# Kernel tuning notes

Measured on AMD Instinct MI355X. Metric: run time of the kernel, lower is better.

The kernel has to match this reference:

```python
import jax, jax.numpy as jnp
import numpy as np

D_MODEL = 1024
NHEAD = 16
HEAD_DIM = D_MODEL // NHEAD
SF_THRESHOLD = 4.0
SF_LEVELS = 8
STEP = SF_THRESHOLD / SF_LEVELS  # quantization step of ScaleAndFireNeuron
EPS = 1e-6


def setup_inputs() -> dict:
    key = jax.random.key(0)
    ks = jax.random.split(key, 12)
    B, L, D = 2, 2048, D_MODEL
    s = 1.0 / np.sqrt(D)
    inp = {
        "x": jax.random.normal(ks[0], (B, L, D), dtype=jnp.float32),
        "wq": jax.random.normal(ks[1], (D, D), dtype=jnp.float32) * s,
        "bq": jnp.zeros((D,), dtype=jnp.float32),
        "wk": jax.random.normal(ks[2], (D, D), dtype=jnp.float32) * s,
        "bk": jnp.zeros((D,), dtype=jnp.float32),
        "wv": jax.random.normal(ks[3], (D, D), dtype=jnp.float32) * s,
        "bv": jnp.zeros((D,), dtype=jnp.float32),
        "wo": jax.random.normal(ks[4], (D, D), dtype=jnp.float32) * s,
        "bo": jnp.zeros((D,), dtype=jnp.float32),
        "gq": jnp.ones((HEAD_DIM,), dtype=jnp.float32),  # SpikingQKNorm gain (q)
        "gk": jnp.ones((HEAD_DIM,), dtype=jnp.float32),  # SpikingQKNorm gain (k)
    }
    return inp


def _rms_norm(t, g):
    # SpikingQKNorm: RMS normalization over head_dim with learned gain
    return t * jax.lax.rsqrt(jnp.mean(t * t, axis=-1, keepdims=True) + EPS) * g


def _sfn(t):
    # ScaleAndFireNeuron: T=1 multi-level spike quantization with straight-through estimator.
    # Levels are integer multiples of STEP, clipped to +/- SF_LEVELS.
    q = jnp.clip(jnp.round(t / STEP), -SF_LEVELS, SF_LEVELS) * STEP
    return t + jax.lax.stop_gradient(q - t)


def reference(x, wq, bq, wk, bk, wv, bv, wo, bo, gq, gk):
    B, L, D = x.shape
    H, Dh = NHEAD, HEAD_DIM
    scale = Dh ** -0.5

    def proj(w, b):
        return (x @ w.T + b).reshape(B, L, H, Dh).transpose(0, 2, 1, 3)  # [B,H,L,Dh]

    q = _sfn(_rms_norm(proj(wq, bq), gq))
    k = _sfn(_rms_norm(proj(wk, bk), gk))
    v = _sfn(proj(wv, bv))

    scores = jnp.einsum('bhqd,bhkd->bhqk', q, k) * scale  # [B,H,L,L]
    probs = jax.nn.softmax(scores, axis=-1)
    out = jnp.einsum('bhqk,bhkd->bhqd', probs, v)  # [B,H,L,Dh]
    out = out.transpose(0, 2, 1, 3).reshape(B, L, D)
    return out @ wo.T + bo
```

## Files before the change

### kernel.cpp

```cpp
#include <hip/hip_runtime.h>
#include <stdint.h>

#define D_MODEL 1024
#define NHEAD 16
#define HEAD_DIM 64
#define SEQ 2048
#define BATCH 2
#define MROWS (BATCH*SEQ)
#define KVBLK 128
#define KVTILES (SEQ/KVBLK)

typedef unsigned short u16;
typedef short bf16x8 __attribute__((ext_vector_type(8)));
typedef float f32x4 __attribute__((ext_vector_type(4)));
typedef float f32x16 __attribute__((ext_vector_type(16)));

__device__ inline float bf2f(u16 h){ return __uint_as_float(((unsigned)h)<<16); }
__device__ inline u16 f2bf(float x){
  unsigned u = __float_as_uint(x);
  unsigned r = (u + 0x7FFFu + ((u>>16)&1u)) >> 16;
  return (u16)r;
}

__device__ inline f32x4 mfma_bf16(bf16x8 a, bf16x8 b, f32x4 c){
  return __builtin_amdgcn_mfma_f32_16x16x32_bf16(a, b, c, 0, 0, 0);
}
__device__ inline f32x16 mfma32_bf16(bf16x8 a, bf16x8 b, f32x16 c){
  return __builtin_amdgcn_mfma_f32_32x32x16_bf16(a, b, c, 0, 0, 0);
}

__device__ inline void gld_lds16(const u16* g, u16* l){
  __builtin_amdgcn_global_load_lds(
      (const __attribute__((address_space(1))) void*)g,
      (__attribute__((address_space(3))) void*)l, 16, 0, 0);
}

__device__ inline int swz8(int row){ return (row ^ (row >> 3)) & 7; }

__device__ inline uint32_t pack_bf2(float p0, float p1){
  uint32_t u0 = __float_as_uint(p0) + 0x8000u;
  uint32_t u1 = __float_as_uint(p1) + 0x8000u;
  return __builtin_amdgcn_perm(u1, u0, 0x07060302u);
}

__global__ __launch_bounds__(256) void pack_split(const float* __restrict__ src,
                                                  u16* __restrict__ hi, u16* __restrict__ lo, int n4){
  int i = blockIdx.x*256 + threadIdx.x;
  if (i >= n4) return;
  float4 v = ((const float4*)src)[i];
  float vv[4] = {v.x, v.y, v.z, v.w};
  u16 h[4], l[4];
  #pragma unroll
  for (int j=0;j<4;j++){
    h[j] = f2bf(vv[j]);
    l[j] = f2bf(vv[j] - bf2f(h[j]));
  }
  ((ushort4*)hi)[i] = make_ushort4(h[0],h[1],h[2],h[3]);
  ((ushort4*)lo)[i] = make_ushort4(l[0],l[1],l[2],l[3]);
}

__global__ __launch_bounds__(256) void pack_w(const float* __restrict__ wq, const float* __restrict__ wk,
                                              const float* __restrict__ wv, const float* __restrict__ wo,
                                              u16* __restrict__ qkv_hi, u16* __restrict__ qkv_lo,
                                              u16* __restrict__ wo_hi, u16* __restrict__ wo_lo){
  int which = blockIdx.x >> 10;
  int i = ((blockIdx.x & 1023) << 8) + threadIdx.x;
  const float* src = which==0 ? wq : which==1 ? wk : which==2 ? wv : wo;
  u16* hi = (which==3) ? wo_hi : qkv_hi + ((size_t)which << 20);
  u16* lo = (which==3) ? wo_lo : qkv_lo + ((size_t)which << 20);
  float4 v = ((const float4*)src)[i];
  float vv[4] = {v.x, v.y, v.z, v.w};
  u16 h[4], l[4];
  #pragma unroll
  for (int j=0;j<4;j++){
    h[j] = f2bf(vv[j]);
    l[j] = f2bf(vv[j] - bf2f(h[j]));
  }
  ((ushort4*)hi)[i] = make_ushort4(h[0],h[1],h[2],h[3]);
  ((ushort4*)lo)[i] = make_ushort4(l[0],l[1],l[2],l[3]);
}

__global__ __launch_bounds__(512) void gemm_qkv(
    const u16* __restrict__ a_hi, const u16* __restrict__ a_lo,
    const u16* __restrict__ b_hi, const u16* __restrict__ b_lo,
    const float* __restrict__ bq, const float* __restrict__ bk_,
    const float* __restrict__ bv,
    u16* __restrict__ qb, u16* __restrict__ kb, u16* __restrict__ vb,
    const float* __restrict__ gq, const float* __restrict__ gk)
{
  __shared__ u16 ldsq[4][16384];
  const int tid = threadIdx.x;
  const int lane = tid & 63;
  const int w = tid >> 6;
  const int wr = w >> 2, wc = w & 3;
  const int l15 = lane & 15;
  const int m0 = blockIdx.x * 256;
  const int n0 = blockIdx.y * 256;
  const int NT = 96;

  f32x4 acc[8][4];
  #pragma unroll
  for (int i=0;i<8;i++)
    #pragma unroll
    for (int j=0;j<4;j++) acc[i][j] = (f32x4){0.f,0.f,0.f,0.f};

  auto stageq = [&](int t){
    u16* base = &ldsq[t & 3][0];
    const u16* As = ((t>>5)==1) ? a_lo : a_hi;
    const u16* Bs = ((t>>5)==2) ? b_lo : b_hi;
    const int kk = (t & 31) << 5;
    #pragma unroll
    for (int r2=0;r2<2;r2++){
      int idx = tid + r2*512;
      int row = idx >> 2, s = idx & 3;
      int g = s ^ ((row >> 1) & 3);
      gld_lds16(As + (size_t)(m0+row)*1024 + kk + (g<<3), base + (idx<<3));
    }
    #pragma unroll
    for (int r2=0;r2<2;r2++){
      int idx = tid + r2*512;
      int row = idx >> 2, s = idx & 3;
      int g = s ^ ((row >> 1) & 3);
      gld_lds16(Bs + (size_t)(n0+row)*1024 + kk + (g<<3), base + 8192 + (idx<<3));
    }
  };

  const int slot = ((lane >> 4) ^ ((l15 >> 1) & 3)) << 3;

  stageq(0); stageq(1);
  asm volatile("s_waitcnt vmcnt(4)" ::: "memory");
  __builtin_amdgcn_s_barrier();

  for (int t=0; t<NT; ++t){
    if (t+2 < NT) stageq(t+2);
    const u16* la = &ldsq[t & 3][0];
    const u16* lb = &ldsq[t & 3][8192];
    bf16x8 af[8], bfr[4];
    #pragma unroll
    for (int mf=0;mf<8;mf++)
      af[mf] = *(const bf16x8*)&la[(wr*128 + mf*16 + l15)*32 + slot];
    #pragma unroll
    for (int nf=0;nf<4;nf++)
      bfr[nf] = *(const bf16x8*)&lb[(wc*64 + nf*16 + l15)*32 + slot];
    __builtin_amdgcn_s_setprio(1);
    #pragma unroll
    for (int mf=0;mf<8;mf++)
      #pragma unroll
      for (int nf=0;nf<4;nf++)
        acc[mf][nf] = mfma_bf16(af[mf], bfr[nf], acc[mf][nf]);
    __builtin_amdgcn_s_setprio(0);
    if (t+1 < NT){
      if (t+2 < NT) asm volatile("s_waitcnt vmcnt(4)" ::: "memory");
      else          asm volatile("s_waitcnt vmcnt(0)" ::: "memory");
      __builtin_amdgcn_s_barrier();
    }
  }

  const int gcolbase = n0 + wc*64;
  const int sidx = gcolbase >> 6;
  const int ttype = sidx < 16 ? 0 : (sidx < 32 ? 1 : 2);
  u16* dst = ttype==0 ? qb : (ttype==1 ? kb : vb);
  const float* bsrc = ttype==0 ? bq : (ttype==1 ? bk_ : bv);
  const int h = sidx - (ttype==1 ? 16 : (ttype==2 ? 32 : 0));
  float gvals[4], bvals[4];
  #pragma unroll
  for (int j=0;j<4;j++){
    int dh = j*16 + l15;
    bvals[j] = bsrc[(gcolbase & 1023) + dh];
    gvals[j] = ttype==0 ? gq[dh] : (ttype==1 ? gk[dh] : 1.0f);
  }
  #pragma unroll
  for (int mf=0;mf<8;mf++){
    #pragma unroll
    for (int r=0;r<4;r++){
      float tv[4];
      float ssq = 0.f;
      #pragma unroll
      for (int j=0;j<4;j++){ tv[j] = acc[mf][j][r] + bvals[j]; ssq += tv[j]*tv[j]; }
      ssq += __shfl_xor(ssq, 1);
      ssq += __shfl_xor(ssq, 2);
      ssq += __shfl_xor(ssq, 4);
      ssq += __shfl_xor(ssq, 8);
      float s = 1.0f;
      if (ttype < 2) s = 1.0f / sqrtf(ssq * (1.0f/64.0f) + 1e-6f);
      int row = m0 + wr*128 + mf*16 + (lane>>4)*4 + r;
      int bi = row >> 11, li = row & 2047;
      size_t obase = ((size_t)(bi*NHEAD + h)*SEQ + li)*HEAD_DIM;
      #pragma unroll
      for (int j=0;j<4;j++){
        float val = tv[j] * s * gvals[j];
        float z = rintf(val * 2.0f);
        z = fminf(8.0f, fmaxf(-8.0f, z));
        dst[obase + j*16 + l15] = f2bf(z * 0.5f);
      }
    }
  }
}

__global__ __launch_bounds__(256) void gemm_bt(
    const u16* __restrict__ a_hi, const u16* __restrict__ b_hi,
    const float* __restrict__ bias, float* __restrict__ out_f,
    int M, int N, int K)
{
  __shared__ u16 lds[2][8192];
  const int tid = threadIdx.x;
  const int lane = tid & 63;
  const int w = tid >> 6;
  const int wr = w >> 1, wc = w & 1;
  const int m0 = blockIdx.x * 128;
  const int n0 = blockIdx.y * 128;
  const int NT = K / 32;

  f32x4 acc[4][4];
  #pragma unroll
  for (int i=0;i<4;i++)
    #pragma unroll
    for (int j=0;j<4;j++) acc[i][j] = (f32x4){0.f,0.f,0.f,0.f};

  auto stage = [&](int buf, int kt){
    int kk = kt * 32;
    u16* base = &lds[buf][0];
    #pragma unroll
    for (int r=0;r<2;r++){
      const u16* g = a_hi + (size_t)(m0 + (tid>>2) + r*64)*K + kk + (tid&3)*8;
      gld_lds16(g, base + w*512 + r*2048);
    }
    #pragma unroll
    for (int r=0;r<2;r++){
      const u16* g = b_hi + (size_t)(n0 + (tid>>2) + r*64)*K + kk + (tid&3)*8;
      gld_lds16(g, base + 4096 + w*512 + r*2048);
    }
  };

  stage(0, 0);
  for (int kt=0; kt<NT; ++kt){
    __syncthreads();
    if (kt+1 < NT) stage((kt+1)&1, kt+1);
    const u16* la = &lds[kt&1][0];
    const u16* lb = &lds[kt&1][4096];
    const int koff = (lane>>4)*8;
    const int rowa = wr*64 + (lane&15);
    const int rowb = wc*64 + (lane&15);
    bf16x8 af[4], bfv[4];
    #pragma unroll
    for (int i=0;i<4;i++) af[i]  = *(const bf16x8*)&la[(rowa + i*16)*32 + koff];
    #pragma unroll
    for (int i=0;i<4;i++) bfv[i] = *(const bf16x8*)&lb[(rowb + i*16)*32 + koff];
    #pragma unroll
    for (int i=0;i<4;i++)
      #pragma unroll
      for (int j=0;j<4;j++)
        acc[i][j] = mfma_bf16(af[i], bfv[j], acc[i][j]);
  }

  const int gcolbase = n0 + wc*64;
  #pragma unroll
  for (int j=0;j<4;j++){
    float bj = bias[gcolbase + j*16 + (lane&15)];
    #pragma unroll
    for (int i=0;i<4;i++){
      int row = m0 + wr*64 + i*16 + (lane>>4)*4;
      #pragma unroll
      for (int r=0;r<4;r++)
        out_f[(size_t)(row+r)*N + gcolbase + j*16 + (lane&15)] = acc[i][j][r] + bj;
    }
  }
}

__global__ __launch_bounds__(256) void transpose_v(const u16* __restrict__ v, u16* __restrict__ vt){
  __shared__ u16 tl[64][66];
  int bh = blockIdx.x >> 5;
  int l0 = (blockIdx.x & 31) * 64;
  int tid = threadIdx.x;
  #pragma unroll
  for (int it=0; it<2; ++it){
    int idx = tid + it*256;
    int row = idx >> 3, g = idx & 7;
    bf16x8 d = *(const bf16x8*)(v + ((size_t)bh*SEQ + l0 + row)*64 + g*8);
    #pragma unroll
    for (int j=0;j<8;j++) tl[row][g*8+j] = (u16)d[j];
  }
  __syncthreads();
  #pragma unroll
  for (int it=0; it<2; ++it){
    int idx = tid + it*256;
    int dh = idx >> 3, g = idx & 7;
    u16 tmp[8];
    #pragma unroll
    for (int j=0;j<8;j++) tmp[j] = tl[g*8+j][dh];
    *(bf16x8*)(vt + ((size_t)bh*HEAD_DIM + dh)*SEQ + l0 + g*8) = *(const bf16x8*)tmp;
  }
}

__global__ __launch_bounds__(256) void attn_kernel(
    const u16* __restrict__ qb, const u16* __restrict__ kb, const u16* __restrict__ vt,
    u16* __restrict__ attn_out)
{
  __shared__ u16 lds_k[2][KVBLK*64];
  __shared__ u16 lds_v[2][64*KVBLK];
  const int tid = threadIdx.x, lane = tid & 63, w = tid >> 6;
  const int bh = blockIdx.y;
  const int q0 = blockIdx.x * 128;
  const size_t kvbase = (size_t)bh * SEQ * HEAD_DIM;
  const size_t vtbase = (size_t)bh * HEAD_DIM * SEQ;
  const int l31 = lane & 31, hi = lane >> 5;

  bf16x8 qf[4];
  #pragma unroll
  for (int kd=0; kd<4; kd++){
    const u16* g = qb + kvbase + (size_t)(q0 + w*32 + l31)*64 + kd*16 + hi*8;
    bf16x8 v = *(const bf16x8*)g;
    #pragma unroll
    for (int j=0;j<8;j++) ((u16*)&v)[j] = f2bf(bf2f((u16)v[j]) * 0.125f);
    qf[kd] = v;
  }

  float m_s = -3.0e38f, l_s = 0.f;
  f32x16 o0, o1;
  #pragma unroll
  for (int r=0;r<16;r++){ o0[r] = 0.f; o1[r] = 0.f; }

  auto stage = [&](int buf, int t){
    const int kv0 = t * KVBLK;
    #pragma unroll
    for (int r=0;r<4;r++){
      int idx = tid + r*256;
      int row = idx >> 3, grp = idx & 7;
      const u16* g = kb + kvbase + (size_t)(kv0 + row)*64 + ((grp ^ swz8(row))<<3);
      gld_lds16(g, &lds_k[buf][idx<<3]);
    }
    #pragma unroll
    for (int r=0;r<4;r++){
      int idx = tid + r*256;
      int row = idx >> 4, grp = idx & 15;
      const u16* g = vt + vtbase + (size_t)row*SEQ + kv0 + ((grp ^ swz8(row))<<3);
      gld_lds16(g, &lds_v[buf][idx<<3]);
    }
  };

  stage(0, 0);
  for (int t=0; t<KVTILES; ++t){
    __syncthreads();
    if (t+1 < KVTILES) stage((t+1)&1, t+1);
    const int buf = t & 1;

    #pragma unroll
    for (int half=0; half<2; ++half){
      f32x16 s0, s1;
      #pragma unroll
      for (int r=0;r<16;r++){ s0[r] = 0.f; s1[r] = 0.f; }
      const int row0 = half*64 + l31;
      const int row1 = half*64 + 32 + l31;
      __builtin_amdgcn_s_setprio(1);
      #pragma unroll
      for (int kd=0; kd<4; kd++){
        bf16x8 a0 = *(const bf16x8*)&lds_k[buf][row0*64 + (((kd*2+hi) ^ swz8(row0))<<3)];
        bf16x8 a1 = *(const bf16x8*)&lds_k[buf][row1*64 + (((kd*2+hi) ^ swz8(row1))<<3)];
        s0 = mfma32_bf16(a0, qf[kd], s0);
        s1 = mfma32_bf16(a1, qf[kd], s1);
      }
      __builtin_amdgcn_s_setprio(0);

      float pmax = s0[0];
      #pragma unroll
      for (int r=1;r<16;r++) pmax = fmaxf(pmax, s0[r]);
      #pragma unroll
      for (int r=0;r<16;r++) pmax = fmaxf(pmax, s1[r]);
      pmax = fmaxf(pmax, __shfl_xor(pmax, 32));

      if (__any(pmax - m_s > 8.0f)) {
        float mnew = fmaxf(m_s, pmax);
        float c = __expf(m_s - mnew);
        m_s = mnew;
        l_s *= c;
        #pragma unroll
        for (int r=0;r<16;r++){
          float cr = __shfl(c, (r&3) + 8*(r>>2) + 4*hi);
          o0[r] *= cr; o1[r] *= cr;
        }
      }

      float rsum = 0.f;
      #pragma unroll
      for (int r=0;r<16;r++){ float p = __expf(s0[r] - m_s); s0[r] = p; rsum += p; }
      #pragma unroll
      for (int r=0;r<16;r++){ float p = __expf(s1[r] - m_s); s1[r] = p; rsum += p; }
      rsum += __shfl_xor(rsum, 32);
      l_s += rsum;

      uint32_t W[2][4][2];
      #pragma unroll
      for (int g=0; g<4; g++){
        W[0][g][0] = pack_bf2(s0[g*4+0], s0[g*4+1]);
        W[0][g][1] = pack_bf2(s0[g*4+2], s0[g*4+3]);
        W[1][g][0] = pack_bf2(s1[g*4+0], s1[g*4+1]);
        W[1][g][1] = pack_bf2(s1[g*4+2], s1[g*4+3]);
      }
      bf16x8 pa[4];
      #pragma unroll
      for (int ks=0; ks<4; ks++){
        const int kvb = ks >> 1, ks0 = ks & 1;
        uint32_t own0 = hi ? W[kvb][ks0*2+1][0] : W[kvb][ks0*2][0];
        uint32_t own1 = hi ? W[kvb][ks0*2+1][1] : W[kvb][ks0*2][1];
        uint32_t t0   = hi ? W[kvb][ks0*2][0]   : W[kvb][ks0*2+1][0];
        uint32_t t1   = hi ? W[kvb][ks0*2][1]   : W[kvb][ks0*2+1][1];
        uint32_t sw0  = (uint32_t)__shfl_xor((int)t0, 32);
        uint32_t sw1  = (uint32_t)__shfl_xor((int)t1, 32);
        uint32_t words[4];
        words[0] = hi ? sw0 : own0;
        words[1] = hi ? sw1 : own1;
        words[2] = hi ? own0 : sw0;
        words[3] = hi ? own1 : sw1;
        pa[ks] = *(const bf16x8*)words;
      }

      __builtin_amdgcn_s_setprio(1);
      #pragma unroll
      for (int ks=0; ks<4; ks++){
        const int rv0 = l31, rv1 = 32 + l31;
        const int cg = half*8 + ks*2 + hi;
        bf16x8 vb0 = *(const bf16x8*)&lds_v[buf][rv0*KVBLK + ((cg ^ swz8(rv0))<<3)];
        bf16x8 vb1 = *(const bf16x8*)&lds_v[buf][rv1*KVBLK + ((cg ^ swz8(rv1))<<3)];
        o0 = mfma32_bf16(pa[ks], vb0, o0);
        o1 = mfma32_bf16(pa[ks], vb1, o1);
      }
      __builtin_amdgcn_s_setprio(0);
    }
  }

  const int b = bh >> 4, h = bh & 15;
  #pragma unroll
  for (int r=0;r<16;r++){
    int q = (r&3) + 8*(r>>2) + 4*hi;
    float linv = 1.0f / __shfl(l_s, q);
    int row = q0 + w*32 + q;
    size_t obase = ((size_t)b*SEQ + row)*D_MODEL + h*64;
    attn_out[obase + l31]      = f2bf(o0[r] * linv);
    attn_out[obase + 32 + l31] = f2bf(o1[r] * linv);
  }
}

extern "C" void kernel_launch(void* const* d_in, const int* in_sizes, int n_in,
                              void* d_out, int out_size, void* d_ws, size_t ws_size,
                              hipStream_t stream){
  const float* x  = (const float*)d_in[0];
  const float* wq = (const float*)d_in[1];
  const float* bq = (const float*)d_in[2];
  const float* wk = (const float*)d_in[3];
  const float* bk = (const float*)d_in[4];
  const float* wv = (const float*)d_in[5];
  const float* bv = (const float*)d_in[6];
  const float* wo = (const float*)d_in[7];
  const float* bo = (const float*)d_in[8];
  const float* gq = (const float*)d_in[9];
  const float* gk = (const float*)d_in[10];
  float* out = (float*)d_out;

  char* ws = (char*)d_ws;
  size_t off = 0;
  auto alloc = [&](size_t bytes) -> char* {
    char* p = ws + off; off += (bytes + 255) & ~(size_t)255; return p;
  };
  const size_t ND = (size_t)MROWS * D_MODEL;
  u16* x_hi    = (u16*)alloc(ND*2);
  u16* x_lo    = (u16*)alloc(ND*2);
  u16* wqkv_hi = (u16*)alloc((size_t)3072*1024*2);
  u16* wqkv_lo = (u16*)alloc((size_t)3072*1024*2);
  u16* wo_hi   = (u16*)alloc((size_t)1024*1024*2);
  u16* wo_lo   = (u16*)alloc((size_t)1024*1024*2);
  u16* q_bf    = (u16*)alloc(ND*2);
  u16* k_bf    = (u16*)alloc(ND*2);
  u16* v_bf    = (u16*)alloc(ND*2);
  u16* vT      = (u16*)alloc(ND*2);
  u16* attn_bf = (u16*)alloc(ND*2);
  (void)ws_size; (void)in_sizes; (void)n_in; (void)out_size;

  pack_split<<<4096, 256, 0, stream>>>(x, x_hi, x_lo, (int)(ND/4));
  pack_w<<<4096, 256, 0, stream>>>(wq, wk, wv, wo, wqkv_hi, wqkv_lo, wo_hi, wo_lo);

  gemm_qkv<<<dim3(16,12), 512, 0, stream>>>(x_hi, x_lo, wqkv_hi, wqkv_lo,
        bq, bk, bv, q_bf, k_bf, v_bf, gq, gk);

  transpose_v<<<1024, 256, 0, stream>>>(v_bf, vT);

  attn_kernel<<<dim3(16,32), 256, 0, stream>>>(q_bf, k_bf, vT, attn_bf);

  gemm_bt<<<dim3(32,8), 256, 0, stream>>>(attn_bf, wo_hi, bo, out, MROWS, 1024, 1024);
}
```

Baseline: 183.9 us.

## Restructure QKV GEMM into 8-wave ping-pong pipeline with grid swizzle

Reworks the QKV projection GEMM main loop. Each iteration now covers a K=64 step, split into four sub-phases that interleave LDS fragment reads, async global-to-LDS staging of one quarter-tile, and MFMA bursts separated by barriers, using two double buffers instead of four rotating ones. This is meant to overlap memory loads with matrix math at finer granularity. The launch also becomes a 1D grid with a block-index swizzle that groups tiles for better L2 reuse of the A and B panels. The cost is many more barriers per iteration and tricky vmcnt accounting, which could stall or be wrong at the pipeline tail.

```diff
diff --git a/kernel.cpp b/kernel.cpp
--- a/kernel.cpp
+++ b/kernel.cpp
@@ -88,15 +88,17 @@
     u16* __restrict__ qb, u16* __restrict__ kb, u16* __restrict__ vb,
     const float* __restrict__ gq, const float* __restrict__ gk)
 {
-  __shared__ u16 ldsq[4][16384];
+  __shared__ u16 lds8[2][32768];
   const int tid = threadIdx.x;
   const int lane = tid & 63;
   const int w = tid >> 6;
   const int wr = w >> 2, wc = w & 3;
   const int l15 = lane & 15;
-  const int m0 = blockIdx.x * 256;
-  const int n0 = blockIdx.y * 256;
-  const int NT = 96;
+  const int orig = blockIdx.x;
+  const int swz = (orig & 7) * 24 + (orig >> 3);
+  const int m0 = (swz & 15) * 256;
+  const int n0 = (swz >> 4) * 256;
+  const int NT = 48;
 
   f32x4 acc[8][4];
   #pragma unroll
@@ -104,56 +106,107 @@
     #pragma unroll
     for (int j=0;j<4;j++) acc[i][j] = (f32x4){0.f,0.f,0.f,0.f};
 
-  auto stageq = [&](int t){
-    u16* base = &ldsq[t & 3][0];
-    const u16* As = ((t>>5)==1) ? a_lo : a_hi;
-    const u16* Bs = ((t>>5)==2) ? b_lo : b_hi;
-    const int kk = (t & 31) << 5;
+  auto stage = [&](int buf, int region, int tt){
+    const int pass = tt >> 4;
+    const u16* src = (region < 2) ? (pass==1 ? a_lo : a_hi)
+                                  : (pass==2 ? b_lo : b_hi);
+    const int base0 = (region < 2) ? m0 : n0;
+    const int kk = ((tt & 15) << 6) + ((region & 1) << 5);
+    u16* dst = &lds8[buf][region << 13];
     #pragma unroll
     for (int r2=0;r2<2;r2++){
-      int idx = tid + r2*512;
+      int idx = tid + (r2<<9);
       int row = idx >> 2, s = idx & 3;
       int g = s ^ ((row >> 1) & 3);
-      gld_lds16(As + (size_t)(m0+row)*1024 + kk + (g<<3), base + (idx<<3));
-    }
-    #pragma unroll
-    for (int r2=0;r2<2;r2++){
-      int idx = tid + r2*512;
-      int row = idx >> 2, s = idx & 3;
-      int g = s ^ ((row >> 1) & 3);
-      gld_lds16(Bs + (size_t)(n0+row)*1024 + kk + (g<<3), base + 8192 + (idx<<3));
+      gld_lds16(src + (size_t)(base0+row)*1024 + kk + (g<<3), dst + (idx<<3));
     }
   };
 
   const int slot = ((lane >> 4) ^ ((l15 >> 1) & 3)) << 3;
-
-  stageq(0); stageq(1);
+  const int arow = wr*128 + l15;
+  const int brow = wc*64  + l15;
+
+  stage(0,0,0); stage(0,1,0); stage(0,2,0); stage(0,3,0);
+  stage(1,0,1); stage(1,2,1);
   asm volatile("s_waitcnt vmcnt(4)" ::: "memory");
   __builtin_amdgcn_s_barrier();
 
   for (int t=0; t<NT; ++t){
-    if (t+2 < NT) stageq(t+2);
-    const u16* la = &ldsq[t & 3][0];
-    const u16* lb = &ldsq[t & 3][8192];
-    bf16x8 af[8], bfr[4];
-    #pragma unroll
-    for (int mf=0;mf<8;mf++)
-      af[mf] = *(const bf16x8*)&la[(wr*128 + mf*16 + l15)*32 + slot];
-    #pragma unroll
-    for (int nf=0;nf<4;nf++)
-      bfr[nf] = *(const bf16x8*)&lb[(wc*64 + nf*16 + l15)*32 + slot];
+    const int buf = t & 1, obuf = buf ^ 1;
+    const u16* A0 = &lds8[buf][0];
+    const u16* A1 = &lds8[buf][8192];
+    const u16* B0 = &lds8[buf][16384];
+    const u16* B1 = &lds8[buf][24576];
+    const bool tail = (t >= NT-2);
+    bf16x8 af[8], bfa, bfb;
+
+    #pragma unroll
+    for (int mf=0;mf<8;mf++) af[mf] = *(const bf16x8*)&A0[(arow+mf*16)*32 + slot];
+    bfa = *(const bf16x8*)&B0[(brow+ 0)*32 + slot];
+    bfb = *(const bf16x8*)&B0[(brow+16)*32 + slot];
+    if (t+1 < NT) stage(obuf, 1, t+1);
+    if (!tail) asm volatile("s_waitcnt vmcnt(8)" ::: "memory");
+    else       asm volatile("s_waitcnt vmcnt(0)" ::: "memory");
+    __builtin_amdgcn_s_barrier();
+    asm volatile("s_waitcnt lgkmcnt(0)" ::: "memory");
     __builtin_amdgcn_s_setprio(1);
     #pragma unroll
-    for (int mf=0;mf<8;mf++)
-      #pragma unroll
-      for (int nf=0;nf<4;nf++)
-        acc[mf][nf] = mfma_bf16(af[mf], bfr[nf], acc[mf][nf]);
+    for (int mf=0;mf<8;mf++){
+      acc[mf][0] = mfma_bf16(af[mf], bfa, acc[mf][0]);
+      acc[mf][1] = mfma_bf16(af[mf], bfb, acc[mf][1]);
+    }
     __builtin_amdgcn_s_setprio(0);
-    if (t+1 < NT){
-      if (t+2 < NT) asm volatile("s_waitcnt vmcnt(4)" ::: "memory");
-      else          asm volatile("s_waitcnt vmcnt(0)" ::: "memory");
-      __builtin_amdgcn_s_barrier();
-    }
+    __builtin_amdgcn_s_barrier();
+
+    bfa = *(const bf16x8*)&B0[(brow+32)*32 + slot];
+    bfb = *(const bf16x8*)&B0[(brow+48)*32 + slot];
+    if (t+1 < NT) stage(obuf, 3, t+1);
+    if (!tail) asm volatile("s_waitcnt vmcnt(8)" ::: "memory");
+    else       asm volatile("s_waitcnt vmcnt(0)" ::: "memory");
+    __builtin_amdgcn_s_barrier();
+    asm volatile("s_waitcnt lgkmcnt(0)" ::: "memory");
+    __builtin_amdgcn_s_setprio(1);
+    #pragma unroll
+    for (int mf=0;mf<8;mf++){
+      acc[mf][2] = mfma_bf16(af[mf], bfa, acc[mf][2]);
+      acc[mf][3] = mfma_bf16(af[mf], bfb, acc[mf][3]);
+    }
+    __builtin_amdgcn_s_setprio(0);
+    __builtin_amdgcn_s_barrier();
+
+    #pragma unroll
+    for (int mf=0;mf<8;mf++) af[mf] = *(const bf16x8*)&A1[(arow+mf*16)*32 + slot];
+    bfa = *(const bf16x8*)&B1[(brow+ 0)*32 + slot];
+    bfb = *(const bf16x8*)&B1[(brow+16)*32 + slot];
+    if (t+2 < NT) stage(buf, 0, t+2);
+    if (!tail) asm volatile("s_waitcnt vmcnt(8)" ::: "memory");
+    else       asm volatile("s_waitcnt vmcnt(0)" ::: "memory");
+    __builtin_amdgcn_s_barrier();
+    asm volatile("s_waitcnt lgkmcnt(0)" ::: "memory");
+    __builtin_amdgcn_s_setprio(1);
+    #pragma unroll
+    for (int mf=0;mf<8;mf++){
+      acc[mf][0] = mfma_bf16(af[mf], bfa, acc[mf][0]);
+      acc[mf][1] = mfma_bf16(af[mf], bfb, acc[mf][1]);
+    }
+    __builtin_amdgcn_s_setprio(0);
+    __builtin_amdgcn_s_barrier();
+
+    bfa = *(const bf16x8*)&B1[(brow+32)*32 + slot];
+    bfb = *(const bf16x8*)&B1[(brow+48)*32 + slot];
+    if (t+2 < NT) stage(buf, 2, t+2);
+    if (!tail) asm volatile("s_waitcnt vmcnt(8)" ::: "memory");
+    else       asm volatile("s_waitcnt vmcnt(0)" ::: "memory");
+    __builtin_amdgcn_s_barrier();
+    asm volatile("s_waitcnt lgkmcnt(0)" ::: "memory");
+    __builtin_amdgcn_s_setprio(1);
+    #pragma unroll
+    for (int mf=0;mf<8;mf++){
+      acc[mf][2] = mfma_bf16(af[mf], bfa, acc[mf][2]);
+      acc[mf][3] = mfma_bf16(af[mf], bfb, acc[mf][3]);
+    }
+    __builtin_amdgcn_s_setprio(0);
+    __builtin_amdgcn_s_barrier();
   }
 
   const int gcolbase = n0 + wc*64;
@@ -478,7 +531,7 @@
   pack_split<<<4096, 256, 0, stream>>>(x, x_hi, x_lo, (int)(ND/4));
   pack_w<<<4096, 256, 0, stream>>>(wq, wk, wv, wo, wqkv_hi, wqkv_lo, wo_hi, wo_lo);
 
-  gemm_qkv<<<dim3(16,12), 512, 0, stream>>>(x_hi, x_lo, wqkv_hi, wqkv_lo,
+  gemm_qkv<<<192, 512, 0, stream>>>(x_hi, x_lo, wqkv_hi, wqkv_lo,
         bq, bk, bv, q_bf, k_bf, v_bf, gq, gk);
 
   transpose_v<<<1024, 256, 0, stream>>>(v_bf, vT);
```

Measured after the change: 187.4 us. About the same (+1.9%).

## Restructure QKV GEMM main loop into 64-wide K steps with split double buffering

Applied to the files above, without the earlier changes.

The QKV projection GEMM now processes K in 64-element steps (48 iterations instead of 96) using two LDS buffers, each split into two 32-wide halves for A and B. Loads of the next step's second half are issued between the first-half fragment reads and the MFMAs, and the first half of the step after next is staged after compute. The aim is to halve the number of loop iterations and barriers per unit of work while keeping global-to-LDS copies overlapped with MFMA work. In exchange the wait counts and barrier placement become more intricate, so a mistake could cause races, and the extra barriers per iteration could offset the savings.

```diff
diff --git a/kernel.cpp b/kernel.cpp
--- a/kernel.cpp
+++ b/kernel.cpp
@@ -88,7 +88,7 @@
     u16* __restrict__ qb, u16* __restrict__ kb, u16* __restrict__ vb,
     const float* __restrict__ gq, const float* __restrict__ gk)
 {
-  __shared__ u16 ldsq[4][16384];
+  __shared__ u16 lds8[2][32768];
   const int tid = threadIdx.x;
   const int lane = tid & 63;
   const int w = tid >> 6;
@@ -96,7 +96,7 @@
   const int l15 = lane & 15;
   const int m0 = blockIdx.x * 256;
   const int n0 = blockIdx.y * 256;
-  const int NT = 96;
+  const int NT = 48;
 
   f32x4 acc[8][4];
   #pragma unroll
@@ -104,54 +104,81 @@
     #pragma unroll
     for (int j=0;j<4;j++) acc[i][j] = (f32x4){0.f,0.f,0.f,0.f};
 
-  auto stageq = [&](int t){
-    u16* base = &ldsq[t & 3][0];
-    const u16* As = ((t>>5)==1) ? a_lo : a_hi;
-    const u16* Bs = ((t>>5)==2) ? b_lo : b_hi;
-    const int kk = (t & 31) << 5;
+  auto stage = [&](int buf, int region, int tt){
+    const int pass = tt >> 4;
+    const u16* src = (region < 2) ? (pass==1 ? a_lo : a_hi)
+                                  : (pass==2 ? b_lo : b_hi);
+    const int base0 = (region < 2) ? m0 : n0;
+    const int kk = ((tt & 15) << 6) + ((region & 1) << 5);
+    u16* dst = &lds8[buf][region << 13];
     #pragma unroll
     for (int r2=0;r2<2;r2++){
-      int idx = tid + r2*512;
+      int idx = tid + (r2<<9);
       int row = idx >> 2, s = idx & 3;
       int g = s ^ ((row >> 1) & 3);
-      gld_lds16(As + (size_t)(m0+row)*1024 + kk + (g<<3), base + (idx<<3));
-    }
-    #pragma unroll
-    for (int r2=0;r2<2;r2++){
-      int idx = tid + r2*512;
-      int row = idx >> 2, s = idx & 3;
-      int g = s ^ ((row >> 1) & 3);
-      gld_lds16(Bs + (size_t)(n0+row)*1024 + kk + (g<<3), base + 8192 + (idx<<3));
+      gld_lds16(src + (size_t)(base0+row)*1024 + kk + (g<<3), dst + (idx<<3));
     }
   };
 
   const int slot = ((lane >> 4) ^ ((l15 >> 1) & 3)) << 3;
-
-  stageq(0); stageq(1);
-  asm volatile("s_waitcnt vmcnt(4)" ::: "memory");
+  const int arow = wr*128 + l15;
+  const int brow = wc*64  + l15;
+
+  stage(0,0,0); stage(0,2,0);
+  stage(0,1,0); stage(0,3,0);
+  stage(1,0,1); stage(1,2,1);
+  asm volatile("s_waitcnt vmcnt(8)" ::: "memory");
   __builtin_amdgcn_s_barrier();
 
   for (int t=0; t<NT; ++t){
-    if (t+2 < NT) stageq(t+2);
-    const u16* la = &ldsq[t & 3][0];
-    const u16* lb = &ldsq[t & 3][8192];
-    bf16x8 af[8], bfr[4];
+    const int buf = t & 1, obuf = buf ^ 1;
+    const u16* A0 = &lds8[buf][0];
+    const u16* A1 = &lds8[buf][8192];
+    const u16* B0 = &lds8[buf][16384];
+    const u16* B1 = &lds8[buf][24576];
+
+    bf16x8 af0[8], bf0[4];
+    #pragma unroll
+    for (int mf=0;mf<8;mf++) af0[mf] = *(const bf16x8*)&A0[(arow+mf*16)*32 + slot];
+    #pragma unroll
+    for (int nf=0;nf<4;nf++) bf0[nf] = *(const bf16x8*)&B0[(brow+nf*16)*32 + slot];
+    if (t+1 < NT){ stage(obuf, 1, t+1); stage(obuf, 3, t+1); }
+
+    if (t < NT-1) asm volatile("s_waitcnt vmcnt(8)" ::: "memory");
+    else          asm volatile("s_waitcnt vmcnt(0)" ::: "memory");
+    __builtin_amdgcn_s_barrier();
+
+    bf16x8 af1[8];
+    #pragma unroll
+    for (int mf=0;mf<8;mf++) af1[mf] = *(const bf16x8*)&A1[(arow+mf*16)*32 + slot];
+
+    __builtin_amdgcn_s_setprio(1);
     #pragma unroll
     for (int mf=0;mf<8;mf++)
-      af[mf] = *(const bf16x8*)&la[(wr*128 + mf*16 + l15)*32 + slot];
-    #pragma unroll
-    for (int nf=0;nf<4;nf++)
-      bfr[nf] = *(const bf16x8*)&lb[(wc*64 + nf*16 + l15)*32 + slot];
+      #pragma unroll
+      for (int nf=0;nf<4;nf++)
+        acc[mf][nf] = mfma_bf16(af0[mf], bf0[nf], acc[mf][nf]);
+    __builtin_amdgcn_s_setprio(0);
+
+    bf16x8 bf1[4];
+    #pragma unroll
+    for (int nf=0;nf<4;nf++) bf1[nf] = *(const bf16x8*)&B1[(brow+nf*16)*32 + slot];
+
     __builtin_amdgcn_s_setprio(1);
     #pragma unroll
     for (int mf=0;mf<8;mf++)
       #pragma unroll
       for (int nf=0;nf<4;nf++)
-        acc[mf][nf] = mfma_bf16(af[mf], bfr[nf], acc[mf][nf]);
+        acc[mf][nf] = mfma_bf16(af1[mf], bf1[nf], acc[mf][nf]);
     __builtin_amdgcn_s_setprio(0);
-    if (t+1 < NT){
-      if (t+2 < NT) asm volatile("s_waitcnt vmcnt(4)" ::: "memory");
-      else          asm volatile("s_waitcnt vmcnt(0)" ::: "memory");
+
+    __builtin_amdgcn_s_barrier();
+    if (t+2 < NT){
+      stage(buf, 0, t+2); stage(buf, 2, t+2);
+      asm volatile("s_waitcnt vmcnt(8)" ::: "memory");
+      __builtin_amdgcn_s_barrier();
+    } else if (t == NT-2){
+      asm volatile("s_waitcnt vmcnt(4)" ::: "memory");
       __builtin_amdgcn_s_barrier();
     }
   }
```

Result: slower. 202.9 us (+10.3%).
